# Kernel tuning notes

Measured on AMD Instinct MI355X. Metric: run time of the kernel, lower is better.

The kernel has to match this reference:

```python
import math
import jax, jax.numpy as jnp
import numpy as np

NUM_HEADS = 16
WINDOW = 64  # neighbor_size
NEG_INF = -1e30


def setup_inputs() -> dict:
    key = jax.random.key(0)
    ks = jax.random.split(key, 5)
    B, L, D = 2, 2048, 1024
    x = jax.random.normal(ks[0], (B, L, D), dtype=jnp.float32)
    s = 0.02
    Wq = jax.random.normal(ks[1], (D, D), dtype=jnp.float32) * s
    Wk = jax.random.normal(ks[2], (D, D), dtype=jnp.float32) * s
    Wv = jax.random.normal(ks[3], (D, D), dtype=jnp.float32) * s
    Wo = jax.random.normal(ks[4], (D, D), dtype=jnp.float32) * s
    return {
        "x": x, "Wq": Wq, "Wk": Wk, "Wv": Wv, "Wo": Wo,
        "sep_gate": jnp.float32(0.1),
        "align_gate": jnp.float32(0.1),
        "coh_gate": jnp.float32(0.1),
    }


def reference(x, Wq, Wk, Wv, Wo, sep_gate, align_gate, coh_gate):
    B, L, D = x.shape
    H = NUM_HEADS
    hd = D // H
    scale = math.sqrt(hd)

    # projections (torch Linear: y = x @ W.T), split heads -> (B, H, L, hd)
    def proj(W):
        return (x @ W.T).reshape(B, L, H, hd).transpose(0, 2, 1, 3)

    q, k, v = proj(Wq), proj(Wk), proj(Wv)

    # raw scores (B, H, L, L)
    scores = jnp.einsum("bhqd,bhkd->bhqk", q, k) / scale

    # Reynolds rules (applied BEFORE masking, mean over full kv dim, as in source)
    similarity = jax.nn.sigmoid(scores)
    separation = -sep_gate * similarity ** 2
    alignment = align_gate * scores
    score_mean = jnp.mean(scores, axis=-1, keepdims=True)
    cohesion = -coh_gate * jnp.abs(scores - score_mean)
    scores = scores + separation + alignment + cohesion

    # causal sliding-window mask: attend iff 0 <= i - j < WINDOW
    i = jnp.arange(L)[:, None]
    j = jnp.arange(L)[None, :]
    dist = i - j
    masked = (dist < 0) | (dist >= WINDOW)  # (L, L) True = blocked
    scores = jnp.where(masked[None, None, :, :], NEG_INF, scores)

    attn = jax.nn.softmax(scores, axis=-1)  # dropout p=0.0 -> identity
    out = jnp.einsum("bhqk,bhkd->bhqd", attn, v)
    out = out.transpose(0, 2, 1, 3).reshape(B, L, D)
    return out @ Wo.T
```

## Files before the change

kernel.cpp:

```cpp
#include <hip/hip_runtime.h>
#include <math.h>

#define L_SEQ 2048
#define DMODEL 1024
#define HEADS 16
#define HD 64
#define BATCH 2
#define MROWS (BATCH*L_SEQ)
#define KDIM 1024
#define VSTRIDE 2136


typedef short bfrag8 __attribute__((ext_vector_type(8)));
typedef float f32x4f __attribute__((ext_vector_type(4)));
typedef unsigned short ushort8v __attribute__((ext_vector_type(8)));

__device__ __forceinline__ unsigned short f2bf(float f) {
    unsigned u = __float_as_uint(f);
    unsigned r = u + 0x7FFFu + ((u >> 16) & 1u);
    return (unsigned short)(r >> 16);
}
__device__ __forceinline__ float bf2f(unsigned short h) {
    return __uint_as_float(((unsigned)h) << 16);
}

__global__ __launch_bounds__(256) void convert_bf16(
    const float* __restrict__ x, const float* __restrict__ wq,
    const float* __restrict__ wk, const float* __restrict__ wv,
    const float* __restrict__ wo,
    unsigned short* __restrict__ xb, unsigned short* __restrict__ qwb,
    unsigned short* __restrict__ kwb, unsigned short* __restrict__ vwb,
    unsigned short* __restrict__ owb, float* __restrict__ kmean_acc)
{
    const int bid = blockIdx.x;
    if (bid == 4096) {
        float4 z = make_float4(0.f, 0.f, 0.f, 0.f);
        *(float4*)&kmean_acc[threadIdx.x * 8]     = z;
        *(float4*)&kmean_acc[threadIdx.x * 8 + 4] = z;
        return;
    }
    const float* src; unsigned short* dst; size_t base;
    if (bid < 2048) { src = x; dst = xb; base = (size_t)bid * 2048; }
    else {
        const int r = bid - 2048; const int w = r >> 9; const int off = r & 511;
        src = (w==0) ? wq : (w==1) ? wk : (w==2) ? wv : wo;
        dst = (w==0) ? qwb : (w==1) ? kwb : (w==2) ? vwb : owb;
        base = (size_t)off * 2048;
    }
    const size_t idx = base + (size_t)threadIdx.x * 8;
    float4 v0 = *(const float4*)&src[idx];
    float4 v1 = *(const float4*)&src[idx + 4];
    ushort8v o;
    o[0] = f2bf(v0.x); o[1] = f2bf(v0.y); o[2] = f2bf(v0.z); o[3] = f2bf(v0.w);
    o[4] = f2bf(v1.x); o[5] = f2bf(v1.y); o[6] = f2bf(v1.z); o[7] = f2bf(v1.w);
    *(ushort8v*)&dst[idx] = o;
}

#define GBK 64

__global__ void mfma_gemm_qkv(
    const unsigned short* __restrict__ A,
    const unsigned short* __restrict__ W0, const unsigned short* __restrict__ W1,
    const unsigned short* __restrict__ W2,
    unsigned short* __restrict__ qo, unsigned short* __restrict__ ko,
    unsigned short* __restrict__ vo, float* __restrict__ kmean_acc)
{
    __shared__ short As[128*GBK];
    __shared__ short Bs[128*GBK];

    const int tid  = threadIdx.x;
    const int wave = tid >> 6, lane = tid & 63;
    const int m0   = blockIdx.x * 128;
    const int n0g  = blockIdx.y * 128;

    const int which = n0g >> 10;
    const int n0 = n0g & 1023;
    const unsigned short* Wp = (which==0) ? W0 : (which==1) ? W1 : W2;

    const int quad = lane >> 4, lm = lane & 15;
    const int wm = wave >> 1, wn = wave & 1;

    f32x4f acc[4][4] = {};

    const int se   = wave * 2048 + lane * 8;
    const int srow = se >> 6;
    const int scg  = (se & 63) >> 3;
    const int sgcol = ((scg ^ (srow & 7)) << 3);

    for (int k0 = 0; k0 < KDIM; k0 += GBK) {
        __syncthreads();
        #pragma unroll
        for (int i = 0; i < 4; ++i) {
            const int ebase = wave * 2048 + i * 512;
            const int row = srow + i * 8;
            __builtin_amdgcn_global_load_lds(
                (const __attribute__((address_space(1))) void*)(A + (size_t)(m0 + row) * KDIM + k0 + sgcol),
                (__attribute__((address_space(3))) void*)(&As[ebase]), 16, 0, 0);
            __builtin_amdgcn_global_load_lds(
                (const __attribute__((address_space(1))) void*)(Wp + (size_t)(n0 + row) * KDIM + k0 + sgcol),
                (__attribute__((address_space(3))) void*)(&Bs[ebase]), 16, 0, 0);
        }
        __syncthreads();

        #pragma unroll
        for (int kk = 0; kk < 2; ++kk) {
            bfrag8 af[4], bf[4];
            #pragma unroll
            for (int t = 0; t < 4; ++t) {
                const int ar = wm*64 + t*16 + lm;
                af[t] = *(const bfrag8*)&As[ar*GBK + (((kk*4 + quad) ^ (ar & 7)) << 3)];
                const int br = wn*64 + t*16 + lm;
                bf[t] = *(const bfrag8*)&Bs[br*GBK + (((kk*4 + quad) ^ (br & 7)) << 3)];
            }
            #pragma unroll
            for (int mt = 0; mt < 4; ++mt)
                #pragma unroll
                for (int nt = 0; nt < 4; ++nt)
                    acc[mt][nt] = __builtin_amdgcn_mfma_f32_16x16x32_bf16(
                        af[mt], bf[nt], acc[mt][nt], 0, 0, 0);
        }
    }

    if (which == 2) {
        #pragma unroll
        for (int mt = 0; mt < 4; ++mt)
            #pragma unroll
            for (int nt = 0; nt < 4; ++nt) {
                const int gn = n0 + wn*64 + nt*16 + lm;
                const int h = gn >> 6, d = gn & 63;
                const int gm0 = m0 + wm*64 + mt*16 + quad*4;
                const int b = gm0 >> 11, l0 = gm0 & (L_SEQ-1);
                ushort4 o;
                o.x = f2bf(acc[mt][nt][0]); o.y = f2bf(acc[mt][nt][1]);
                o.z = f2bf(acc[mt][nt][2]); o.w = f2bf(acc[mt][nt][3]);
                *(ushort4*)&vo[((size_t)((b*HEADS + h)*HD + d))*VSTRIDE + 64 + l0] = o;
            }
    } else {
        unsigned short* Cp = (which==0) ? qo : ko;
        #pragma unroll
        for (int mt = 0; mt < 4; ++mt)
            #pragma unroll
            for (int nt = 0; nt < 4; ++nt) {
                const int gn = n0 + wn*64 + nt*16 + lm;
                const int h = gn >> 6, d = gn & 63;
                #pragma unroll
                for (int r = 0; r < 4; ++r) {
                    const int gm = m0 + wm*64 + mt*16 + quad*4 + r;
                    const int b = gm >> 11, l = gm & (L_SEQ-1);
                    Cp[(((size_t)(b*HEADS + h) * L_SEQ) + l) * HD + d] = f2bf(acc[mt][nt][r]);
                }
            }
        if (which == 1) {
            const int b = m0 >> 11;
            #pragma unroll
            for (int nt = 0; nt < 4; ++nt) {
                const int gn = n0 + wn*64 + nt*16 + lm;
                const int h = gn >> 6, d = gn & 63;
                float s = 0.f;
                #pragma unroll
                for (int mt = 0; mt < 4; ++mt)
                    #pragma unroll
                    for (int r = 0; r < 4; ++r) s += acc[mt][nt][r];
                s += __shfl_xor(s, 16, 64);
                s += __shfl_xor(s, 32, 64);
                if (quad == 0)
                    atomicAdd(&kmean_acc[(size_t)(b*HEADS + h)*HD + d], s);
            }
        }
    }
}

__global__ void out_proj_gemm(
    const unsigned short* __restrict__ A, const unsigned short* __restrict__ W,
    float* __restrict__ C)
{
    __shared__ short As[64*GBK];
    __shared__ short Bs[128*GBK];

    const int tid  = threadIdx.x;
    const int wave = tid >> 6, lane = tid & 63;
    const int m0   = blockIdx.x * 64;
    const int n0   = blockIdx.y * 128;

    const int quad = lane >> 4, lm = lane & 15;
    const int wm = wave >> 1, wn = wave & 1;

    f32x4f acc[2][4] = {};

    const int sea   = wave * 1024 + lane * 8;
    const int srowa = sea >> 6;
    const int sga   = ((((sea & 63) >> 3) ^ (srowa & 7)) << 3);
    const int seb   = wave * 2048 + lane * 8;
    const int srowb = seb >> 6;
    const int sgb   = ((((seb & 63) >> 3) ^ (srowb & 7)) << 3);

    for (int k0 = 0; k0 < KDIM; k0 += GBK) {
        __syncthreads();
        #pragma unroll
        for (int i = 0; i < 2; ++i) {
            const int ebase = wave * 1024 + i * 512;
            const int row = srowa + i * 8;
            __builtin_amdgcn_global_load_lds(
                (const __attribute__((address_space(1))) void*)(A + (size_t)(m0 + row) * KDIM + k0 + sga),
                (__attribute__((address_space(3))) void*)(&As[ebase]), 16, 0, 0);
        }
        #pragma unroll
        for (int i = 0; i < 4; ++i) {
            const int ebase = wave * 2048 + i * 512;
            const int row = srowb + i * 8;
            __builtin_amdgcn_global_load_lds(
                (const __attribute__((address_space(1))) void*)(W + (size_t)(n0 + row) * KDIM + k0 + sgb),
                (__attribute__((address_space(3))) void*)(&Bs[ebase]), 16, 0, 0);
        }
        __syncthreads();

        #pragma unroll
        for (int kk = 0; kk < 2; ++kk) {
            bfrag8 af[2], bf[4];
            #pragma unroll
            for (int t = 0; t < 2; ++t) {
                const int ar = wm*32 + t*16 + lm;
                af[t] = *(const bfrag8*)&As[ar*GBK + (((kk*4 + quad) ^ (ar & 7)) << 3)];
            }
            #pragma unroll
            for (int t = 0; t < 4; ++t) {
                const int br = wn*64 + t*16 + lm;
                bf[t] = *(const bfrag8*)&Bs[br*GBK + (((kk*4 + quad) ^ (br & 7)) << 3)];
            }
            #pragma unroll
            for (int mt = 0; mt < 2; ++mt)
                #pragma unroll
                for (int nt = 0; nt < 4; ++nt)
                    acc[mt][nt] = __builtin_amdgcn_mfma_f32_16x16x32_bf16(
                        af[mt], bf[nt], acc[mt][nt], 0, 0, 0);
        }
    }

    #pragma unroll
    for (int mt = 0; mt < 2; ++mt)
        #pragma unroll
        for (int nt = 0; nt < 4; ++nt) {
            const int gn = n0 + wn*64 + nt*16 + lm;
            #pragma unroll
            for (int r = 0; r < 4; ++r) {
                const int gm = m0 + wm*32 + mt*16 + quad*4 + r;
                C[(size_t)gm * DMODEL + gn] = acc[mt][nt][r];
            }
        }
}

#define P_STRIDE 104

__global__ __launch_bounds__(256) void attn_kernel(
    const unsigned short* __restrict__ qb, const unsigned short* __restrict__ kb,
    const unsigned short* __restrict__ vt, const float* __restrict__ kmean_acc,
    const float* __restrict__ g_sep, const float* __restrict__ g_align,
    const float* __restrict__ g_coh, unsigned short* __restrict__ out)
{
    __shared__ unsigned short pl[64 * P_STRIDE];

    const int tid = threadIdx.x;
    const int bh = blockIdx.x >> 5;
    const int qt = blockIdx.x & 31;
    const int q0 = qt * 64;
    const int j0 = q0 - 64;

    const int w = tid >> 6, lane = tid & 63;
    const int quad = lane >> 4, lm = lane & 15;
    const float sep = g_sep[0], align = g_align[0], coh = g_coh[0];

    const unsigned short* kbh = kb + (size_t)bh * L_SEQ * HD;
    const unsigned short* vbh = vt + (size_t)bh * HD * VSTRIDE;

    const unsigned short* qrow =
        qb + ((size_t)bh * L_SEQ + q0 + w*16 + lm) * HD + quad * 8;
    bfrag8 qa0 = *(const bfrag8*)qrow;
    bfrag8 qa1 = *(const bfrag8*)(qrow + 32);

    const float* kmp = kmean_acc + bh * HD + quad * 8;
    float4 km0 = *(const float4*)(kmp);
    float4 km1 = *(const float4*)(kmp + 4);
    float4 km2 = *(const float4*)(kmp + 32);
    float4 km3 = *(const float4*)(kmp + 36);
    float part =
        bf2f((unsigned short)qa0[0])*km0.x + bf2f((unsigned short)qa0[1])*km0.y +
        bf2f((unsigned short)qa0[2])*km0.z + bf2f((unsigned short)qa0[3])*km0.w +
        bf2f((unsigned short)qa0[4])*km1.x + bf2f((unsigned short)qa0[5])*km1.y +
        bf2f((unsigned short)qa0[6])*km1.z + bf2f((unsigned short)qa0[7])*km1.w +
        bf2f((unsigned short)qa1[0])*km2.x + bf2f((unsigned short)qa1[1])*km2.y +
        bf2f((unsigned short)qa1[2])*km2.z + bf2f((unsigned short)qa1[3])*km2.w +
        bf2f((unsigned short)qa1[4])*km3.x + bf2f((unsigned short)qa1[5])*km3.y +
        bf2f((unsigned short)qa1[6])*km3.z + bf2f((unsigned short)qa1[7])*km3.w;
    part *= (1.f / (float)L_SEQ);
    part += __shfl_xor(part, 16, 64);
    part += __shfl_xor(part, 32, 64);

    f32x4f sacc[6];
    #pragma unroll
    for (int t = 0; t < 6; ++t) {
        int kr = j0 + w*16 + t*16 + lm;
        kr = kr < 0 ? 0 : (kr >= L_SEQ ? L_SEQ - 1 : kr);
        const unsigned short* kp = kbh + (size_t)kr * HD + quad * 8;
        bfrag8 b0 = *(const bfrag8*)kp;
        bfrag8 b1 = *(const bfrag8*)(kp + 32);
        f32x4f z = {0.f, 0.f, 0.f, 0.f};
        z = __builtin_amdgcn_mfma_f32_16x16x32_bf16(qa0, b0, z, 0, 0, 0);
        sacc[t] = __builtin_amdgcn_mfma_f32_16x16x32_bf16(qa1, b1, z, 0, 0, 0);
    }

    float rinv[4];
    #pragma unroll
    for (int r = 0; r < 4; ++r) {
        const int row = quad*4 + r;
        const int i   = q0 + w*16 + row;
        const float mean_i = __shfl(part, row, 64) * 0.125f;
        float sc[6]; float mx = -3.0e38f;
        #pragma unroll
        for (int t = 0; t < 6; ++t) {
            const int jabs = j0 + w*16 + t*16 + lm;
            const int dist = i - jabs;
            float s = sacc[t][r] * 0.125f;
            const float sig = 1.f / (1.f + __expf(-s));
            float adj = s * (1.f + align) - sep * sig * sig - coh * fabsf(s - mean_i);
            const bool ok = (dist >= 0) && (dist < 64) && (jabs >= 0);
            sc[t] = ok ? adj : -3.0e38f;
            mx = fmaxf(mx, sc[t]);
        }
        mx = fmaxf(mx, __shfl_xor(mx, 1, 64));
        mx = fmaxf(mx, __shfl_xor(mx, 2, 64));
        mx = fmaxf(mx, __shfl_xor(mx, 4, 64));
        mx = fmaxf(mx, __shfl_xor(mx, 8, 64));
        float ls = 0.f;
        #pragma unroll
        for (int t = 0; t < 6; ++t) {
            const float p = __expf(sc[t] - mx);
            ls += p;
            pl[(w*16 + row) * P_STRIDE + t*16 + lm] = f2bf(p);
        }
        ls += __shfl_xor(ls, 1, 64);
        ls += __shfl_xor(ls, 2, 64);
        ls += __shfl_xor(ls, 4, 64);
        ls += __shfl_xor(ls, 8, 64);
        rinv[r] = 1.f / ls;
    }

    f32x4f oacc[4] = {};
    #pragma unroll
    for (int kk = 0; kk < 3; ++kk) {
        bfrag8 pa = *(const bfrag8*)&pl[(w*16 + lm) * P_STRIDE + kk*32 + quad*8];
        const int loff = 64 + j0 + w*16 + kk*32 + quad*8;
        #pragma unroll
        for (int nt = 0; nt < 4; ++nt) {
            bfrag8 bv = *(const bfrag8*)&vbh[(size_t)(nt*16 + lm) * VSTRIDE + loff];
            oacc[nt] = __builtin_amdgcn_mfma_f32_16x16x32_bf16(pa, bv, oacc[nt], 0, 0, 0);
        }
    }

    const int b = bh >> 4, h = bh & (HEADS - 1);
    #pragma unroll
    for (int nt = 0; nt < 4; ++nt)
        #pragma unroll
        for (int r = 0; r < 4; ++r) {
            const int i = q0 + w*16 + quad*4 + r;
            const int d = nt*16 + lm;
            out[((size_t)(b * L_SEQ + i)) * DMODEL + h * HD + d] =
                f2bf(oacc[nt][r] * rinv[r]);
        }
}

extern "C" void kernel_launch(void* const* d_in, const int* in_sizes, int n_in,
                              void* d_out, int out_size, void* d_ws, size_t ws_size,
                              hipStream_t stream)
{
    (void)in_sizes; (void)n_in; (void)out_size; (void)ws_size;
    const float* x     = (const float*)d_in[0];
    const float* Wq    = (const float*)d_in[1];
    const float* Wk    = (const float*)d_in[2];
    const float* Wv    = (const float*)d_in[3];
    const float* Wo    = (const float*)d_in[4];
    const float* g_sep   = (const float*)d_in[5];
    const float* g_align = (const float*)d_in[6];
    const float* g_coh   = (const float*)d_in[7];
    float* out = (float*)d_out;

    float* kmean_ws = (float*)d_ws;
    unsigned short* xb  = (unsigned short*)(kmean_ws + 2048);
    const size_t per = (size_t)MROWS * DMODEL;
    unsigned short* wqb = xb  + per;
    unsigned short* wkb = wqb + (size_t)DMODEL*KDIM;
    unsigned short* wvb = wkb + (size_t)DMODEL*KDIM;
    unsigned short* wob = wvb + (size_t)DMODEL*KDIM;
    unsigned short* qb  = wob + (size_t)DMODEL*KDIM;
    unsigned short* kb  = qb  + per;
    unsigned short* vtb = kb  + per;
    unsigned short* attb = vtb + (size_t)BATCH*HEADS*HD*VSTRIDE;

    convert_bf16<<<dim3(4097), dim3(256), 0, stream>>>(
        x, Wq, Wk, Wv, Wo, xb, wqb, wkb, wvb, wob, kmean_ws);
    mfma_gemm_qkv<<<dim3(MROWS/128, 3*DMODEL/128), dim3(256), 0, stream>>>(
        xb, wqb, wkb, wvb, qb, kb, vtb, kmean_ws);
    attn_kernel<<<dim3(BATCH*HEADS*(L_SEQ/64)), dim3(256), 0, stream>>>(
        qb, kb, vtb, kmean_ws, g_sep, g_align, g_coh, attb);
    out_proj_gemm<<<dim3(MROWS/64, DMODEL/128), dim3(256), 0, stream>>>(
        attb, wob, out);
}
```

Measured before the change: 148.6 us.

## Enlarge QKV GEMM tile to 256x192 with 512 threads over concatenated weights

The fused QKV projection GEMM moves from 128x128 tiles with 256 threads to 256x192 tiles with 512 threads (8 waves, each computing 64x96). The three weight matrices are indexed as one contiguous 3072-row matrix, which relies on wq/wk/wv being adjacent in the workspace, and Q/K/V routing is chosen per 16-column fragment in the epilogue. The larger tile reuses each LDS load across more MFMAs and halves the grid to 256 blocks. In exchange it uses more registers (24 accumulators per lane), more LDS, and the grid may fill the CUs less evenly.

New measurement: 157.1 us. +5.7%, slower.

```diff
diff --git a/kernel.cpp b/kernel.cpp
--- a/kernel.cpp
+++ b/kernel.cpp
@@ -58,104 +58,102 @@
 
 #define GBK 64
 
-__global__ void mfma_gemm_qkv(
+__global__ __launch_bounds__(512, 2) void mfma_gemm_qkv(
     const unsigned short* __restrict__ A,
-    const unsigned short* __restrict__ W0, const unsigned short* __restrict__ W1,
-    const unsigned short* __restrict__ W2,
+    const unsigned short* __restrict__ W,
     unsigned short* __restrict__ qo, unsigned short* __restrict__ ko,
     unsigned short* __restrict__ vo, float* __restrict__ kmean_acc)
 {
-    __shared__ short As[128*GBK];
-    __shared__ short Bs[128*GBK];
+    __shared__ short As[256*GBK];
+    __shared__ short Bs[192*GBK];
 
     const int tid  = threadIdx.x;
     const int wave = tid >> 6, lane = tid & 63;
-    const int m0   = blockIdx.x * 128;
-    const int n0g  = blockIdx.y * 128;
-
-    const int which = n0g >> 10;
-    const int n0 = n0g & 1023;
-    const unsigned short* Wp = (which==0) ? W0 : (which==1) ? W1 : W2;
-
     const int quad = lane >> 4, lm = lane & 15;
     const int wm = wave >> 1, wn = wave & 1;
 
-    f32x4f acc[4][4] = {};
-
-    const int se   = wave * 2048 + lane * 8;
-    const int srow = se >> 6;
-    const int scg  = (se & 63) >> 3;
-    const int sgcol = ((scg ^ (srow & 7)) << 3);
+    const int m0  = blockIdx.x * 256;
+    const int n0g = blockIdx.y * 192;
+
+    const int rla = lane >> 3;
+    const int cg  = lane & 7;
+    const int sra = wave*32 + rla;
+    const int srb = wave*24 + rla;
+
+    f32x4f acc[4][6] = {};
 
     for (int k0 = 0; k0 < KDIM; k0 += GBK) {
         __syncthreads();
         #pragma unroll
         for (int i = 0; i < 4; ++i) {
-            const int ebase = wave * 2048 + i * 512;
-            const int row = srow + i * 8;
+            const int row = sra + i*8;
             __builtin_amdgcn_global_load_lds(
-                (const __attribute__((address_space(1))) void*)(A + (size_t)(m0 + row) * KDIM + k0 + sgcol),
-                (__attribute__((address_space(3))) void*)(&As[ebase]), 16, 0, 0);
+                (const __attribute__((address_space(1))) void*)(A + (size_t)(m0 + row) * KDIM + k0 + ((cg ^ (row & 7)) << 3)),
+                (__attribute__((address_space(3))) void*)(&As[wave*2048 + i*512]), 16, 0, 0);
+        }
+        #pragma unroll
+        for (int i = 0; i < 3; ++i) {
+            const int row = srb + i*8;
             __builtin_amdgcn_global_load_lds(
-                (const __attribute__((address_space(1))) void*)(Wp + (size_t)(n0 + row) * KDIM + k0 + sgcol),
-                (__attribute__((address_space(3))) void*)(&Bs[ebase]), 16, 0, 0);
+                (const __attribute__((address_space(1))) void*)(W + (size_t)(n0g + row) * KDIM + k0 + ((cg ^ (row & 7)) << 3)),
+                (__attribute__((address_space(3))) void*)(&Bs[wave*1536 + i*512]), 16, 0, 0);
         }
         __syncthreads();
 
         #pragma unroll
         for (int kk = 0; kk < 2; ++kk) {
-            bfrag8 af[4], bf[4];
+            bfrag8 af[4], bf[6];
             #pragma unroll
             for (int t = 0; t < 4; ++t) {
                 const int ar = wm*64 + t*16 + lm;
                 af[t] = *(const bfrag8*)&As[ar*GBK + (((kk*4 + quad) ^ (ar & 7)) << 3)];
-                const int br = wn*64 + t*16 + lm;
+            }
+            #pragma unroll
+            for (int t = 0; t < 6; ++t) {
+                const int br = (2*t + wn)*16 + lm;
                 bf[t] = *(const bfrag8*)&Bs[br*GBK + (((kk*4 + quad) ^ (br & 7)) << 3)];
             }
             #pragma unroll
             for (int mt = 0; mt < 4; ++mt)
                 #pragma unroll
-                for (int nt = 0; nt < 4; ++nt)
+                for (int nt = 0; nt < 6; ++nt)
                     acc[mt][nt] = __builtin_amdgcn_mfma_f32_16x16x32_bf16(
                         af[mt], bf[nt], acc[mt][nt], 0, 0, 0);
         }
     }
 
-    if (which == 2) {
-        #pragma unroll
-        for (int mt = 0; mt < 4; ++mt)
-            #pragma unroll
-            for (int nt = 0; nt < 4; ++nt) {
-                const int gn = n0 + wn*64 + nt*16 + lm;
-                const int h = gn >> 6, d = gn & 63;
+    const int bq = m0 >> 11;
+    #pragma unroll
+    for (int nt = 0; nt < 6; ++nt) {
+        const int fn  = 2*nt + wn;
+        const int gng = n0g + fn*16 + lm;
+        const int which = gng >> 10;
+        const int gn = gng & 1023;
+        const int h = gn >> 6, d = gn & 63;
+        if (which == 2) {
+            #pragma unroll
+            for (int mt = 0; mt < 4; ++mt) {
                 const int gm0 = m0 + wm*64 + mt*16 + quad*4;
-                const int b = gm0 >> 11, l0 = gm0 & (L_SEQ-1);
+                const int l0  = gm0 & (L_SEQ-1);
+                const f32x4f a = acc[mt][nt];
                 ushort4 o;
-                o.x = f2bf(acc[mt][nt][0]); o.y = f2bf(acc[mt][nt][1]);
-                o.z = f2bf(acc[mt][nt][2]); o.w = f2bf(acc[mt][nt][3]);
-                *(ushort4*)&vo[((size_t)((b*HEADS + h)*HD + d))*VSTRIDE + 64 + l0] = o;
-            }
-    } else {
-        unsigned short* Cp = (which==0) ? qo : ko;
-        #pragma unroll
-        for (int mt = 0; mt < 4; ++mt)
-            #pragma unroll
-            for (int nt = 0; nt < 4; ++nt) {
-                const int gn = n0 + wn*64 + nt*16 + lm;
-                const int h = gn >> 6, d = gn & 63;
+                o.x = f2bf(a[0]); o.y = f2bf(a[1]);
+                o.z = f2bf(a[2]); o.w = f2bf(a[3]);
+                *(ushort4*)&vo[((size_t)((bq*HEADS + h)*HD + d))*VSTRIDE + 64 + l0] = o;
+            }
+        } else {
+            unsigned short* Cp = (which==0) ? qo : ko;
+            #pragma unroll
+            for (int mt = 0; mt < 4; ++mt) {
+                const f32x4f a = acc[mt][nt];
                 #pragma unroll
                 for (int r = 0; r < 4; ++r) {
                     const int gm = m0 + wm*64 + mt*16 + quad*4 + r;
-                    const int b = gm >> 11, l = gm & (L_SEQ-1);
-                    Cp[(((size_t)(b*HEADS + h) * L_SEQ) + l) * HD + d] = f2bf(acc[mt][nt][r]);
+                    const int l = gm & (L_SEQ-1);
+                    Cp[(((size_t)(bq*HEADS + h) * L_SEQ) + l) * HD + d] = f2bf(a[r]);
                 }
             }
-        if (which == 1) {
-            const int b = m0 >> 11;
-            #pragma unroll
-            for (int nt = 0; nt < 4; ++nt) {
-                const int gn = n0 + wn*64 + nt*16 + lm;
-                const int h = gn >> 6, d = gn & 63;
+            if (which == 1) {
                 float s = 0.f;
                 #pragma unroll
                 for (int mt = 0; mt < 4; ++mt)
@@ -164,7 +162,7 @@
                 s += __shfl_xor(s, 16, 64);
                 s += __shfl_xor(s, 32, 64);
                 if (quad == 0)
-                    atomicAdd(&kmean_acc[(size_t)(b*HEADS + h)*HD + d], s);
+                    atomicAdd(&kmean_acc[(size_t)(bq*HEADS + h)*HD + d], s);
             }
         }
     }
@@ -397,8 +395,8 @@
 
     convert_bf16<<<dim3(4097), dim3(256), 0, stream>>>(
         x, Wq, Wk, Wv, Wo, xb, wqb, wkb, wvb, wob, kmean_ws);
-    mfma_gemm_qkv<<<dim3(MROWS/128, 3*DMODEL/128), dim3(256), 0, stream>>>(
-        xb, wqb, wkb, wvb, qb, kb, vtb, kmean_ws);
+    mfma_gemm_qkv<<<dim3(16, 16), dim3(512), 0, stream>>>(
+        xb, wqb, qb, kb, vtb, kmean_ws);
     attn_kernel<<<dim3(BATCH*HEADS*(L_SEQ/64)), dim3(256), 0, stream>>>(
         qb, kb, vtb, kmean_ws, g_sep, g_align, g_coh, attb);
     out_proj_gemm<<<dim3(MROWS/64, DMODEL/128), dim3(256), 0, stream>>>(
```

## Load weight fragments directly from global memory and remap QKV block order

Applied to the files above, without the earlier changes.

Both GEMMs stop staging the weight tile in shared memory and have each wave read its B fragments straight from global memory into registers. The QKV GEMM also remaps its block indices so that consecutive blocks share weight tiles, to improve L2 reuse. The intent is to cut shared-memory traffic and LDS footprint, which may raise occupancy. In exchange, every wave now issues its own global loads, the pair of waves sharing a column range (wm=0 and wm=1) fetch the same data twice, and the loads are no longer overlapped with the async LDS copy, so global latency may be exposed.

Result: slower. 195.8 us (+31.8%).

```diff
diff --git a/kernel.cpp b/kernel.cpp
--- a/kernel.cpp
+++ b/kernel.cpp
@@ -66,12 +66,14 @@
     unsigned short* __restrict__ vo, float* __restrict__ kmean_acc)
 {
     __shared__ short As[128*GBK];
-    __shared__ short Bs[128*GBK];
 
     const int tid  = threadIdx.x;
     const int wave = tid >> 6, lane = tid & 63;
-    const int m0   = blockIdx.x * 128;
-    const int n0g  = blockIdx.y * 128;
+
+    const int raw = blockIdx.x + blockIdx.y * 32;
+    const int sid = (raw & 7) * 96 + (raw >> 3);
+    const int m0   = (sid & 31) * 128;
+    const int n0g  = (sid >> 5) * 128;
 
     const int which = n0g >> 10;
     const int n0 = n0g & 1023;
@@ -86,6 +88,11 @@
     const int srow = se >> 6;
     const int scg  = (se & 63) >> 3;
     const int sgcol = ((scg ^ (srow & 7)) << 3);
+
+    const unsigned short* Wrow[4];
+    #pragma unroll
+    for (int t = 0; t < 4; ++t)
+        Wrow[t] = Wp + (size_t)(n0 + wn*64 + t*16 + lm) * KDIM;
 
     for (int k0 = 0; k0 < KDIM; k0 += GBK) {
         __syncthreads();
@@ -96,9 +103,6 @@
             __builtin_amdgcn_global_load_lds(
                 (const __attribute__((address_space(1))) void*)(A + (size_t)(m0 + row) * KDIM + k0 + sgcol),
                 (__attribute__((address_space(3))) void*)(&As[ebase]), 16, 0, 0);
-            __builtin_amdgcn_global_load_lds(
-                (const __attribute__((address_space(1))) void*)(Wp + (size_t)(n0 + row) * KDIM + k0 + sgcol),
-                (__attribute__((address_space(3))) void*)(&Bs[ebase]), 16, 0, 0);
         }
         __syncthreads();
 
@@ -109,8 +113,7 @@
             for (int t = 0; t < 4; ++t) {
                 const int ar = wm*64 + t*16 + lm;
                 af[t] = *(const bfrag8*)&As[ar*GBK + (((kk*4 + quad) ^ (ar & 7)) << 3)];
-                const int br = wn*64 + t*16 + lm;
-                bf[t] = *(const bfrag8*)&Bs[br*GBK + (((kk*4 + quad) ^ (br & 7)) << 3)];
+                bf[t] = *(const bfrag8*)&Wrow[t][k0 + (kk*4 + quad)*8];
             }
             #pragma unroll
             for (int mt = 0; mt < 4; ++mt)
@@ -175,7 +178,6 @@
     float* __restrict__ C)
 {
     __shared__ short As[64*GBK];
-    __shared__ short Bs[128*GBK];
 
     const int tid  = threadIdx.x;
     const int wave = tid >> 6, lane = tid & 63;
@@ -190,9 +192,11 @@
     const int sea   = wave * 1024 + lane * 8;
     const int srowa = sea >> 6;
     const int sga   = ((((sea & 63) >> 3) ^ (srowa & 7)) << 3);
-    const int seb   = wave * 2048 + lane * 8;
-    const int srowb = seb >> 6;
-    const int sgb   = ((((seb & 63) >> 3) ^ (srowb & 7)) << 3);
+
+    const unsigned short* Wrow[4];
+    #pragma unroll
+    for (int t = 0; t < 4; ++t)
+        Wrow[t] = W + (size_t)(n0 + wn*64 + t*16 + lm) * KDIM;
 
     for (int k0 = 0; k0 < KDIM; k0 += GBK) {
         __syncthreads();
@@ -204,14 +208,6 @@
                 (const __attribute__((address_space(1))) void*)(A + (size_t)(m0 + row) * KDIM + k0 + sga),
                 (__attribute__((address_space(3))) void*)(&As[ebase]), 16, 0, 0);
         }
-        #pragma unroll
-        for (int i = 0; i < 4; ++i) {
-            const int ebase = wave * 2048 + i * 512;
-            const int row = srowb + i * 8;
-            __builtin_amdgcn_global_load_lds(
-                (const __attribute__((address_space(1))) void*)(W + (size_t)(n0 + row) * KDIM + k0 + sgb),
-                (__attribute__((address_space(3))) void*)(&Bs[ebase]), 16, 0, 0);
-        }
         __syncthreads();
 
         #pragma unroll
@@ -223,10 +219,8 @@
                 af[t] = *(const bfrag8*)&As[ar*GBK + (((kk*4 + quad) ^ (ar & 7)) << 3)];
             }
             #pragma unroll
-            for (int t = 0; t < 4; ++t) {
-                const int br = wn*64 + t*16 + lm;
-                bf[t] = *(const bfrag8*)&Bs[br*GBK + (((kk*4 + quad) ^ (br & 7)) << 3)];
-            }
+            for (int t = 0; t < 4; ++t)
+                bf[t] = *(const bfrag8*)&Wrow[t][k0 + (kk*4 + quad)*8];
             #pragma unroll
             for (int mt = 0; mt < 2; ++mt)
                 #pragma unroll
```
